# Optimization experiments

Hardware: AMD Instinct MI355X
Metric: run time of the kernel (lower is better)

The kernel has to match this reference:

```python
import jax, jax.numpy as jnp
import numpy as np
from jax import lax

B, N, NPOINT = 8, 8192, 1024
NSAMPLE = (16, 32)
IN_CH = 64
MLPS = ((64, 64, 128), (64, 96, 128))
EPS = 1e-5


def setup_inputs() -> dict:
    key = jax.random.key(0)
    ks = jax.random.split(key, 16)
    inp = {}
    inp["xyz"] = jax.random.normal(ks[0], (B, 3, N), jnp.float32)
    inp["points"] = jax.random.normal(ks[1], (B, IN_CH, N), jnp.float32)
    ki = 2
    for i, mlp in enumerate(MLPS):
        last = IN_CH + 3
        for j, out in enumerate(mlp):
            inp["w%d_%d" % (i, j)] = jax.random.normal(ks[ki], (out, last), jnp.float32) * (1.0 / float(np.sqrt(last)))
            inp["b%d_%d" % (i, j)] = jnp.zeros((out,), jnp.float32)
            inp["g%d_%d" % (i, j)] = jnp.ones((out,), jnp.float32)
            inp["be%d_%d" % (i, j)] = jnp.zeros((out,), jnp.float32)
            ki += 1
            last = out
    return inp


def _fps(xyz_t):
    # farthest point sampling; xyz_t: [B, N, 3] -> [B, NPOINT] int32
    Bb, Nn, _ = xyz_t.shape

    def step(carry, _):
        dist, far = carry
        c = jnp.take_along_axis(xyz_t, far[:, None, None], axis=1)  # [B,1,3]
        d = jnp.sum((xyz_t - c) ** 2, -1)
        dist = jnp.minimum(dist, d)
        return (dist, jnp.argmax(dist, -1).astype(jnp.int32)), far

    init = (jnp.full((Bb, Nn), 1e10, jnp.float32), jnp.zeros((Bb,), jnp.int32))
    _, cent = lax.scan(step, init, None, length=NPOINT)
    return cent.T  # [B, NPOINT]


def _gather(p, idx):
    # p: [B, N, C], idx: [B, ...] -> [B, ..., C]
    return jax.vmap(lambda a, i: a[i])(p, idx)


def _sqdist(a, b):
    # a: [B, S, 3], b: [B, N, 3] -> [B, S, N] squared euclidean distance
    return (jnp.sum(a * a, -1)[:, :, None] + jnp.sum(b * b, -1)[:, None, :]
            - 2.0 * jnp.einsum('bsc,bnc->bsn', a, b))


def _mlp(x, params):
    # x: [B, C, S, K]; 1x1 Conv2d + BatchNorm2d (batch stats, training mode) + ReLU
    for w, b, g, be in params:
        x = jnp.einsum('oc,bcsk->bosk', w, x) + b[None, :, None, None]
        m = x.mean((0, 2, 3), keepdims=True)
        v = x.var((0, 2, 3), keepdims=True)
        x = (x - m) * lax.rsqrt(v + EPS) * g[None, :, None, None] + be[None, :, None, None]
        x = jax.nn.relu(x)
    return x


def _forward(xyz, points, params):
    xyz_t = jnp.transpose(xyz, (0, 2, 1))     # [B, N, 3]
    pts_t = jnp.transpose(points, (0, 2, 1))  # [B, N, C]
    fps_idx = _fps(xyz_t)
    new_xyz = _gather(xyz_t, fps_idx)         # [B, S, 3]
    outs = []
    for i, k in enumerate(NSAMPLE):
        d = _sqdist(new_xyz, xyz_t)           # [B, S, N]
        _, idx = lax.top_k(-d, k)             # k nearest neighbors
        g_xyz = _gather(xyz_t, idx) - new_xyz[:, :, None, :]  # [B, S, k, 3]
        g_pts = _gather(pts_t, idx)                           # [B, S, k, C]
        feat = jnp.transpose(jnp.concatenate([g_xyz, g_pts], -1), (0, 3, 1, 2))  # [B, 3+C, S, k]
        outs.append(jnp.max(_mlp(feat, params[i]), -1))       # [B, C_out, S]
    return jnp.transpose(new_xyz, (0, 2, 1)), jnp.concatenate(outs, 1)


def reference(xyz, points, w0_0, b0_0, g0_0, be0_0, w0_1, b0_1, g0_1, be0_1, w0_2, b0_2, g0_2, be0_2, w1_0, b1_0, g1_0, be1_0, w1_1, b1_1, g1_1, be1_1, w1_2, b1_2, g1_2, be1_2):
    params = [[(w0_0, b0_0, g0_0, be0_0), (w0_1, b0_1, g0_1, be0_1), (w0_2, b0_2, g0_2, be0_2)],
              [(w1_0, b1_0, g1_0, be1_0), (w1_1, b1_1, g1_1, be1_1), (w1_2, b1_2, g1_2, be1_2)]]
    return _forward(xyz, points, params)
```

## Files before the change

kernel.cpp:

```cpp
#include <hip/hip_runtime.h>
#include <math.h>

#define BN_EPS 1e-5f
constexpr int Bc = 8, Nc = 8192, Sc = 1024, CINc = 64;

typedef float v2f __attribute__((ext_vector_type(2)));

__device__ __forceinline__ unsigned short f2bf(float f) {
  unsigned u = __float_as_uint(f);
  u += 0x7FFFu + ((u >> 16) & 1u);
  return (unsigned short)(u >> 16);
}
__device__ __forceinline__ float bf2f(unsigned short h) {
  return __uint_as_float(((unsigned)h) << 16);
}

template <int CTRL, int RMASK>
__device__ __forceinline__ unsigned long long dpp_maxu64(unsigned long long k) {
  int lo = (int)(unsigned)k, hi = (int)(unsigned)(k >> 32);
  int olo = __builtin_amdgcn_update_dpp(lo, lo, CTRL, RMASK, 0xF, false);
  int ohi = __builtin_amdgcn_update_dpp(hi, hi, CTRL, RMASK, 0xF, false);
  unsigned long long ok = ((unsigned long long)(unsigned)ohi << 32) | (unsigned)olo;
  return ok > k ? ok : k;
}
template <int CTRL, int RMASK>
__device__ __forceinline__ v2f dpp_sumstep2(v2f v) {
  int olo = __builtin_amdgcn_update_dpp(0, __float_as_int(v.x), CTRL, RMASK, 0xF, false);
  int ohi = __builtin_amdgcn_update_dpp(0, __float_as_int(v.y), CTRL, RMASK, 0xF, false);
  v2f o = {__int_as_float(olo), __int_as_float(ohi)};
  return v + o;
}
__device__ __forceinline__ v2f dpp_sum64v2(v2f v) {
  v = dpp_sumstep2<0x111, 0xF>(v);
  v = dpp_sumstep2<0x112, 0xF>(v);
  v = dpp_sumstep2<0x114, 0xF>(v);
  v = dpp_sumstep2<0x118, 0xF>(v);
  v = dpp_sumstep2<0x142, 0xA>(v);
  v = dpp_sumstep2<0x143, 0xC>(v);
  return v;
}
template <int CTRL>
__device__ __forceinline__ v2f dpp_pkmax(v2f v) {
  int ox = __builtin_amdgcn_update_dpp(__float_as_int(v.x), __float_as_int(v.x), CTRL, 0xF, 0xF, false);
  int oy = __builtin_amdgcn_update_dpp(__float_as_int(v.y), __float_as_int(v.y), CTRL, 0xF, 0xF, false);
  v2f o = {__int_as_float(ox), __int_as_float(oy)};
  return __builtin_elementwise_max(v, o);
}
template <int CTRL>
__device__ __forceinline__ v2f dpp_pkmin(v2f v) {
  int ox = __builtin_amdgcn_update_dpp(__float_as_int(v.x), __float_as_int(v.x), CTRL, 0xF, 0xF, false);
  int oy = __builtin_amdgcn_update_dpp(__float_as_int(v.y), __float_as_int(v.y), CTRL, 0xF, 0xF, false);
  v2f o = {__int_as_float(ox), __int_as_float(oy)};
  return __builtin_elementwise_min(v, o);
}

__device__ __forceinline__ void pproj_body(int i, const float* __restrict__ pts,
                                           const float* __restrict__ wl,
                                           const float* __restrict__ bl,
                                           float* __restrict__ P) {
  int b = i >> 13, n = i & 8191;
  const float* pb = pts + (size_t)b * CINc * Nc + n;
  v2f acc[32];
  const v2f* bl2 = (const v2f*)bl;
#pragma unroll
  for (int o2 = 0; o2 < 32; o2++) acc[o2] = bl2[o2];
  for (int c = 0; c < CINc; c++) {
    float xv = pb[(size_t)c * Nc];
    v2f xv2 = {xv, xv};
    const v2f* wr = (const v2f*)(wl + c * 64);
#pragma unroll
    for (int o2 = 0; o2 < 32; o2++) acc[o2] = __builtin_elementwise_fma(wr[o2], xv2, acc[o2]);
  }
  float4* Pn = (float4*)(P + (size_t)i * 64);
#pragma unroll
  for (int o4 = 0; o4 < 16; o4++)
    Pn[o4] = make_float4(acc[2 * o4].x, acc[2 * o4].y, acc[2 * o4 + 1].x, acc[2 * o4 + 1].y);
}

__global__ __launch_bounds__(512) void mega_kernel(const float* __restrict__ xyz,
                                                   const float* __restrict__ pts,
                                                   const float* __restrict__ w00,
                                                   const float* __restrict__ b00,
                                                   const float* __restrict__ w10,
                                                   const float* __restrict__ b10,
                                                   float4* __restrict__ xyzT,
                                                   float4* __restrict__ nx,
                                                   float* __restrict__ out0,
                                                   float* __restrict__ P0,
                                                   float* __restrict__ P1) {
  __shared__ alignas(16) char smemc[102528];
  int bid = blockIdx.x, t = threadIdx.x;
  if (bid < 8) {
    float* xs = (float*)smemc;
    float* ys = xs + Nc;
    float* zs = ys + Nc;
    int* idxs = (int*)(smemc + 98304);
    unsigned long long* red = (unsigned long long*)(smemc + 102400);
    const float* xb = xyz + (size_t)bid * 3 * Nc;
    float px[16], py[16], pz[16], dd[16];
#pragma unroll
    for (int j = 0; j < 16; j++) {
      int n = j * 512 + t;
      float x = xb[n], y = xb[Nc + n], z = xb[2 * Nc + n];
      px[j] = x; py[j] = y; pz[j] = z;
      xs[n] = x; ys[n] = y; zs[n] = z;
      dd[j] = 1e10f;
    }
    int w = t >> 6;
    __syncthreads();
    int curIdx = 0;
    for (int i = 0; i < Sc; i++) {
      float cx = xs[curIdx], cy = ys[curIdx], cz = zs[curIdx];
      if (t == 0) idxs[i] = curIdx;
      float bd = -1.f;
      int bnidx = 0;
#pragma unroll
      for (int j = 0; j < 16; j++) {
        float dx = px[j] - cx, dy = py[j] - cy, dz = pz[j] - cz;
        float d = fmaf(dz, dz, fmaf(dy, dy, dx * dx));
        d = fminf(dd[j], d);
        dd[j] = d;
        if (d > bd) { bd = d; bnidx = j * 512 + t; }
      }
      unsigned long long key =
          ((unsigned long long)__float_as_uint(bd) << 32) | (unsigned)(~bnidx);
      key = dpp_maxu64<0x111, 0xF>(key);
      key = dpp_maxu64<0x112, 0xF>(key);
      key = dpp_maxu64<0x114, 0xF>(key);
      key = dpp_maxu64<0x118, 0xF>(key);
      key = dpp_maxu64<0x142, 0xA>(key);
      key = dpp_maxu64<0x143, 0xC>(key);
      if ((t & 63) == 63) red[(i & 1) * 8 + w] = key;
      __syncthreads();
      const unsigned long long* rr = red + (i & 1) * 8;
      unsigned long long k2 = rr[0];
#pragma unroll
      for (int u = 1; u < 8; u++) {
        unsigned long long o = rr[u];
        k2 = (o > k2) ? o : k2;
      }
      curIdx = (int)(~(unsigned)(k2 & 0xFFFFFFFFull));
    }
    __syncthreads();
    for (int i2 = t; i2 < Sc; i2 += 512) {
      int idx = idxs[i2];
      float x = xs[idx], y = ys[idx], z = zs[idx];
      nx[bid * Sc + i2] = make_float4(x, y, z, fmaf(z, z, fmaf(y, y, x * x)));
      float* ob = out0 + (size_t)bid * 3 * Sc;
      ob[i2] = x; ob[Sc + i2] = y; ob[2 * Sc + i2] = z;
    }
  } else if (bid < 136) {
    int i = (bid - 8) * 512 + t;
    int b = i >> 13, n = i & 8191;
    const float* xb = xyz + (size_t)b * 3 * Nc;
    float x = xb[n], y = xb[Nc + n], z = xb[2 * Nc + n];
    xyzT[i] = make_float4(x, y, z, fmaf(z, z, fmaf(y, y, x * x)));
  } else {
    bool second = bid >= 264;
    const float* ww = second ? w10 : w00;
    const float* bb = second ? b10 : b00;
    float* PP = second ? P1 : P0;
    float* wl = (float*)smemc;
    float* bl = wl + 64 * 64;
    for (int i2 = t; i2 < 64 * 64; i2 += 512) {
      int c = i2 >> 6, o = i2 & 63;
      wl[i2] = ww[o * 67 + 3 + c];
    }
    if (t < 64) bl[t] = bb[t];
    __syncthreads();
    pproj_body(((bid - (second ? 264 : 136)) * 512) + t, pts, wl, bl, PP);
  }
}

__global__ __launch_bounds__(256) void knn_kernel(const float4* __restrict__ xyzT,
                                                  const float4* __restrict__ newxyz,
                                                  int* __restrict__ knn) {
  int lane = threadIdx.x & 63;
  int sub = lane >> 5;
  int l32 = lane & 31;
  int waveId = blockIdx.x * 4 + (threadIdx.x >> 6);
  int q = waveId * 2 + sub;
  int b = q >> 10;
  float4 qv = newxyz[q];
  const float4* pb = xyzT + (size_t)b * Nc;
  unsigned long long lk = ~0ull;
  unsigned long long worst = ~0ull;
  for (int t0 = 0; t0 < Nc; t0 += 32) {
    float4 p = pb[t0 + l32];
    float dot = fmaf(qv.z, p.z, fmaf(qv.y, p.y, qv.x * p.x));
    float d = fmaf(-2.f, dot, qv.w + p.w);
    unsigned fu = __float_as_uint(d);
    fu ^= (unsigned)(-(int)(fu >> 31)) | 0x80000000u;
    unsigned long long ck = ((unsigned long long)fu << 32) | (unsigned)(t0 + l32);
    unsigned long long bal = __ballot(ck < worst);
    unsigned mymask = (unsigned)(bal >> (sub * 32));
    while (mymask) {
      int src = __ffs(mymask) - 1;
      unsigned long long ckb = __shfl(ck, src, 32);
      unsigned long long bel = __ballot(lk < ckb);
      int cnt = __popc((unsigned)(bel >> (sub * 32)));
      unsigned long long up = __shfl_up(lk, 1, 32);
      lk = (l32 == cnt) ? ckb : ((l32 > cnt) ? up : lk);
      worst = __shfl(lk, 31, 32);
      mymask &= ~(1u << src);
      unsigned long long bal2 = __ballot(ck < worst);
      mymask &= (unsigned)(bal2 >> (sub * 32));
    }
  }
  knn[(size_t)q * 32 + l32] = (int)(lk & 0xFFFFFFFFu);
}

template <int K>
__device__ __forceinline__ void conv1_body(char* smemc, int bidl,
                                           const float4* __restrict__ xyzT,
                                           const float4* __restrict__ nx,
                                           const int* __restrict__ knn,
                                           const float* __restrict__ P,
                                           const float* __restrict__ w0,
                                           unsigned short* __restrict__ y,
                                           float* __restrict__ part, int Pos) {
  v2f* wst = (v2f*)smemc;
  float* wx = (float*)(smemc + 8192);
  float* wy = wx + 64;
  float* wz = wy + 64;
  if (threadIdx.x < 64) {
    int o = threadIdx.x;
    wx[o] = w0[o * 67];
    wy[o] = w0[o * 67 + 1];
    wz[o] = w0[o * 67 + 2];
  }
  __syncthreads();
  int gp = bidl * 256 + threadIdx.x;
  int b = gp / Pos, r = gp % Pos;
  int s = r / K, kk = r & (K - 1);
  int n = knn[((size_t)(b * Sc + s)) * 32 + kk];
  float4 c4 = nx[b * Sc + s];
  float4 p4 = xyzT[(size_t)b * Nc + n];
  v2f dx2 = {p4.x - c4.x, p4.x - c4.x};
  v2f dy2 = {p4.y - c4.y, p4.y - c4.y};
  v2f dz2 = {p4.z - c4.z, p4.z - c4.z};
  const float4* Pn = (const float4*)(P + ((size_t)b * Nc + n) * 64);
  v2f acc[32];
#pragma unroll
  for (int o4 = 0; o4 < 16; o4++) {
    float4 v = Pn[o4];
    acc[2 * o4] = (v2f){v.x, v.y};
    acc[2 * o4 + 1] = (v2f){v.z, v.w};
  }
  const v2f* wx2 = (const v2f*)wx;
  const v2f* wy2 = (const v2f*)wy;
  const v2f* wz2 = (const v2f*)wz;
#pragma unroll
  for (int o2 = 0; o2 < 32; o2++) acc[o2] = __builtin_elementwise_fma(wx2[o2], dx2, acc[o2]);
#pragma unroll
  for (int o2 = 0; o2 < 32; o2++) acc[o2] = __builtin_elementwise_fma(wy2[o2], dy2, acc[o2]);
#pragma unroll
  for (int o2 = 0; o2 < 32; o2++) acc[o2] = __builtin_elementwise_fma(wz2[o2], dz2, acc[o2]);
  unsigned short* yt = y + (size_t)bidl * 64 * 256 + threadIdx.x;
#pragma unroll
  for (int o2 = 0; o2 < 32; o2++) {
    yt[(size_t)(2 * o2) * 256] = f2bf(acc[o2].x);
    yt[(size_t)(2 * o2 + 1) * 256] = f2bf(acc[o2].y);
  }
  int lane = threadIdx.x & 63, w = threadIdx.x >> 6;
  int row = w * 4 + (lane >> 4);
  bool lead = (lane & 15) == 15;
#pragma unroll
  for (int o2 = 0; o2 < 32; o2++) {
    float v0 = acc[o2].x, v1 = acc[o2].y;
    v2f s0 = (v2f){v0, v0 * v0};
    s0 = dpp_sumstep2<0x111, 0xF>(s0);
    s0 = dpp_sumstep2<0x112, 0xF>(s0);
    s0 = dpp_sumstep2<0x114, 0xF>(s0);
    s0 = dpp_sumstep2<0x118, 0xF>(s0);
    v2f s1 = (v2f){v1, v1 * v1};
    s1 = dpp_sumstep2<0x111, 0xF>(s1);
    s1 = dpp_sumstep2<0x112, 0xF>(s1);
    s1 = dpp_sumstep2<0x114, 0xF>(s1);
    s1 = dpp_sumstep2<0x118, 0xF>(s1);
    if (lead) { wst[row * 64 + 2 * o2] = s0; wst[row * 64 + 2 * o2 + 1] = s1; }
  }
  __syncthreads();
  if (threadIdx.x < 64) {
    int o = threadIdx.x;
    v2f sv = (v2f){0.f, 0.f};
#pragma unroll
    for (int rr = 0; rr < 16; rr++) sv += wst[rr * 64 + o];
    ((v2f*)part)[(size_t)bidl * 64 + o] = sv;
  }
}

__global__ __launch_bounds__(256) void conv1M_kernel(
    const float4* xyzT, const float4* nx, const int* knn,
    const float* P0, const float* w0a, unsigned short* y0a, float* part0, int Pos0,
    const float* P1, const float* w0b, unsigned short* y0b, float* part1, int Pos1, int split) {
  __shared__ alignas(16) char smemc[8960];
  if ((int)blockIdx.x < split)
    conv1_body<16>(smemc, blockIdx.x, xyzT, nx, knn, P0, w0a, y0a, part0, Pos0);
  else
    conv1_body<32>(smemc, blockIdx.x - split, xyzT, nx, knn, P1, w0b, y0b, part1, Pos1);
}

__global__ __launch_bounds__(256) void bnfinM_kernel(
    const float* part0, const float* g0, const float* be0, float* bn0, int C0, int nblk0, float inv0,
    const float* part1, const float* g1, const float* be1, float* bn1, int C1, int nblk1, float inv1,
    int split) {
  const float* part; const float* g; const float* be; float* bn;
  int C, nblk, c; float invcnt;
  if ((int)blockIdx.x < split) {
    part = part0; g = g0; be = be0; bn = bn0; C = C0; nblk = nblk0; invcnt = inv0; c = blockIdx.x;
  } else {
    part = part1; g = g1; be = be1; bn = bn1; C = C1; nblk = nblk1; invcnt = inv1; c = blockIdx.x - split;
  }
  v2f sq = (v2f){0.f, 0.f};
  for (int i = threadIdx.x; i < nblk; i += 256) sq += ((const v2f*)part)[(size_t)i * C + c];
  sq = dpp_sum64v2(sq);
  __shared__ v2f ls[4];
  int w = threadIdx.x >> 6;
  if ((threadIdx.x & 63) == 63) ls[w] = sq;
  __syncthreads();
  if (threadIdx.x == 0) {
    v2f tt = ls[0] + ls[1] + ls[2] + ls[3];
    float m = tt.x * invcnt;
    float v = tt.y * invcnt - m * m;
    float sc = g[c] / sqrtf(v + BN_EPS);
    bn[c * 2] = sc;
    bn[c * 2 + 1] = fmaf(-m, sc, be[c]);
  }
}

template <int CI, int CO, int K>
__device__ __forceinline__ void convB_body(char* smemc, int bidl,
                                           const unsigned short* __restrict__ yin,
                                           const float* __restrict__ wt,
                                           const float* __restrict__ bb,
                                           const float* __restrict__ bn,
                                           unsigned short* __restrict__ yout,
                                           float* __restrict__ ymax,
                                           float* __restrict__ ymin,
                                           float* __restrict__ part, int Pos) {
  constexpr int COq = CO / 4;
  constexpr int COq2 = COq / 2;
  float* wl = (float*)smemc;
  float* bnl = wl + CI * CO;
  float* bl = bnl + 2 * CI;
  for (int i = threadIdx.x; i < CI * CO; i += 256) {
    int c = i / CO, o = i % CO;
    wl[i] = wt[o * CI + c];
  }
  for (int i = threadIdx.x; i < 2 * CI; i += 256) bnl[i] = bn[i];
  if (threadIdx.x < CO) bl[threadIdx.x] = bb[threadIdx.x];
  __syncthreads();
  int w = threadIdx.x >> 6, l = threadIdx.x & 63;
  int cb = w * COq;
  int bpb = Pos / 256;
  int b = bidl / bpb;
  int r0 = (bidl % bpb) * 256 + l * 4;
  const ushort4* xt = (const ushort4*)(yin + (size_t)bidl * CI * 256) + l;
  v2f acc[4][COq2];
#pragma unroll
  for (int p = 0; p < 4; p++)
#pragma unroll
    for (int q = 0; q < COq2; q++) acc[p][q] = ((const v2f*)(bl + cb))[q];
  ushort4 cur = xt[0], nxt;
  for (int c = 0; c < CI; c++) {
    if (c + 1 < CI) nxt = xt[(c + 1) * 64];
    float scv = bnl[2 * c], shv = bnl[2 * c + 1];
    float xv0 = fmaxf(fmaf(bf2f(cur.x), scv, shv), 0.f);
    float xv1 = fmaxf(fmaf(bf2f(cur.y), scv, shv), 0.f);
    float xv2 = fmaxf(fmaf(bf2f(cur.z), scv, shv), 0.f);
    float xv3 = fmaxf(fmaf(bf2f(cur.w), scv, shv), 0.f);
    v2f x0 = {xv0, xv0}, x1 = {xv1, xv1}, x2 = {xv2, xv2}, x3 = {xv3, xv3};
    const float4* wr = (const float4*)(wl + c * CO + cb);
#pragma unroll
    for (int o4 = 0; o4 < COq / 4; o4++) {
      float4 wv = wr[o4];
      v2f w01 = {wv.x, wv.y}, w23 = {wv.z, wv.w};
      acc[0][2 * o4] = __builtin_elementwise_fma(w01, x0, acc[0][2 * o4]);
      acc[0][2 * o4 + 1] = __builtin_elementwise_fma(w23, x0, acc[0][2 * o4 + 1]);
      acc[1][2 * o4] = __builtin_elementwise_fma(w01, x1, acc[1][2 * o4]);
      acc[1][2 * o4 + 1] = __builtin_elementwise_fma(w23, x1, acc[1][2 * o4 + 1]);
      acc[2][2 * o4] = __builtin_elementwise_fma(w01, x2, acc[2][2 * o4]);
      acc[2][2 * o4 + 1] = __builtin_elementwise_fma(w23, x2, acc[2][2 * o4 + 1]);
      acc[3][2 * o4] = __builtin_elementwise_fma(w01, x3, acc[3][2 * o4]);
      acc[3][2 * o4 + 1] = __builtin_elementwise_fma(w23, x3, acc[3][2 * o4 + 1]);
    }
    cur = nxt;
  }
  if (K == 0) {
    unsigned short* yo = yout + (size_t)bidl * CO * 256;
#pragma unroll
    for (int q = 0; q < COq2; q++) {
      ushort4 a, bq;
      a.x = f2bf(acc[0][q].x); a.y = f2bf(acc[1][q].x);
      a.z = f2bf(acc[2][q].x); a.w = f2bf(acc[3][q].x);
      bq.x = f2bf(acc[0][q].y); bq.y = f2bf(acc[1][q].y);
      bq.z = f2bf(acc[2][q].y); bq.w = f2bf(acc[3][q].y);
      ((ushort4*)(yo + (size_t)(cb + 2 * q) * 256))[l] = a;
      ((ushort4*)(yo + (size_t)(cb + 2 * q + 1) * 256))[l] = bq;
    }
  } else {
    int s = r0 / K;
    bool wrt = (K == 16) ? ((l & 3) == 3) : ((l & 7) == 7);
#pragma unroll
    for (int q = 0; q < COq2; q++) {
      v2f mx = __builtin_elementwise_max(__builtin_elementwise_max(acc[0][q], acc[1][q]),
                                         __builtin_elementwise_max(acc[2][q], acc[3][q]));
      v2f mn = __builtin_elementwise_min(__builtin_elementwise_min(acc[0][q], acc[1][q]),
                                         __builtin_elementwise_min(acc[2][q], acc[3][q]));
      mx = dpp_pkmax<0x111>(mx);
      mx = dpp_pkmax<0x112>(mx);
      if (K == 32) mx = dpp_pkmax<0x114>(mx);
      mn = dpp_pkmin<0x111>(mn);
      mn = dpp_pkmin<0x112>(mn);
      if (K == 32) mn = dpp_pkmin<0x114>(mn);
      if (wrt) {
        ymax[((size_t)b * CO + cb + 2 * q) * Sc + s] = mx.x;
        ymax[((size_t)b * CO + cb + 2 * q + 1) * Sc + s] = mx.y;
        ymin[((size_t)b * CO + cb + 2 * q) * Sc + s] = mn.x;
        ymin[((size_t)b * CO + cb + 2 * q + 1) * Sc + s] = mn.y;
      }
    }
  }
#pragma unroll
  for (int q = 0; q < COq2; q++) {
    v2f sv = acc[0][q] + acc[1][q] + acc[2][q] + acc[3][q];
    v2f sq = acc[0][q] * acc[0][q];
    sq = __builtin_elementwise_fma(acc[1][q], acc[1][q], sq);
    sq = __builtin_elementwise_fma(acc[2][q], acc[2][q], sq);
    sq = __builtin_elementwise_fma(acc[3][q], acc[3][q], sq);
    sv = dpp_sum64v2(sv);
    sq = dpp_sum64v2(sq);
    if (l == 63) {
      ((v2f*)part)[(size_t)bidl * CO + cb + 2 * q] = (v2f){sv.x, sq.x};
      ((v2f*)part)[(size_t)bidl * CO + cb + 2 * q + 1] = (v2f){sv.y, sq.y};
    }
  }
}

__global__ __launch_bounds__(256) void conv2M_kernel(
    const unsigned short* y0a, const float* w1a, const float* b1a, const float* bn1a,
    unsigned short* y1a, float* part0, int Pos0,
    const unsigned short* y0b, const float* w1b, const float* b1b, const float* bn1b,
    unsigned short* y1b, float* part1, int Pos1, int split) {
  __shared__ alignas(16) char smemc[25472];
  if ((int)blockIdx.x < split)
    convB_body<64, 64, 0>(smemc, blockIdx.x, y0a, w1a, b1a, bn1a, y1a, nullptr, nullptr, part0, Pos0);
  else
    convB_body<64, 96, 0>(smemc, blockIdx.x - split, y0b, w1b, b1b, bn1b, y1b, nullptr, nullptr, part1, Pos1);
}

__global__ __launch_bounds__(256) void conv3M_kernel(
    const unsigned short* y1a, const float* w2a, const float* b2a, const float* bn2a,
    float* ymax0, float* ymin0, float* part0, int Pos0,
    const unsigned short* y1b, const float* w2b, const float* b2b, const float* bn2b,
    float* ymax1, float* ymin1, float* part1, int Pos1, int split) {
  __shared__ alignas(16) char smemc[50432];
  if ((int)blockIdx.x < split)
    convB_body<64, 128, 16>(smemc, blockIdx.x, y1a, w2a, b2a, bn2a, nullptr, ymax0, ymin0, part0, Pos0);
  else
    convB_body<96, 128, 32>(smemc, blockIdx.x - split, y1b, w2b, b2b, bn2b, nullptr, ymax1, ymin1, part1, Pos1);
}

__global__ __launch_bounds__(256) void bnfin3fM_kernel(
    const float* part0, const float* g0, const float* be0, const float* ymax0,
    const float* ymin0, int nblk0, float inv0, int coff0,
    const float* part1, const float* g1, const float* be1, const float* ymax1,
    const float* ymin1, int nblk1, float inv1, int coff1,
    float* out1, int split) {
  constexpr int C = 128;
  const float* part; const float* g; const float* be; const float* ymaxp; const float* yminp;
  int nblk, c, coff; float invcnt;
  if ((int)blockIdx.x < split) {
    part = part0; g = g0; be = be0; ymaxp = ymax0; yminp = ymin0;
    nblk = nblk0; invcnt = inv0; coff = coff0; c = blockIdx.x;
  } else {
    part = part1; g = g1; be = be1; ymaxp = ymax1; yminp = ymin1;
    nblk = nblk1; invcnt = inv1; coff = coff1; c = blockIdx.x - split;
  }
  v2f sq = (v2f){0.f, 0.f};
  for (int i = threadIdx.x; i < nblk; i += 256) sq += ((const v2f*)part)[(size_t)i * C + c];
  sq = dpp_sum64v2(sq);
  __shared__ v2f ls[4];
  __shared__ float bnc[2];
  int w = threadIdx.x >> 6;
  if ((threadIdx.x & 63) == 63) ls[w] = sq;
  __syncthreads();
  if (threadIdx.x == 0) {
    v2f tt = ls[0] + ls[1] + ls[2] + ls[3];
    float m = tt.x * invcnt;
    float v = tt.y * invcnt - m * m;
    float sc = g[c] / sqrtf(v + BN_EPS);
    bnc[0] = sc;
    bnc[1] = fmaf(-m, sc, be[c]);
  }
  __syncthreads();
  float sc = bnc[0], sh = bnc[1];
  const float* src = (sc >= 0.f) ? ymaxp : yminp;
#pragma unroll
  for (int k = 0; k < 32; k++) {
    int i = k * 256 + threadIdx.x;
    int b = i >> 10, s = i & 1023;
    float v = src[((size_t)b * C + c) * Sc + s];
    out1[((size_t)b * 256 + coff + c) * Sc + s] = fmaxf(fmaf(v, sc, sh), 0.f);
  }
}

extern "C" void kernel_launch(void* const* d_in, const int* in_sizes, int n_in,
                              void* d_out, int out_size, void* d_ws, size_t ws_size,
                              hipStream_t stream) {
  const float* xyz = (const float*)d_in[0];
  const float* pts = (const float*)d_in[1];
  float* ws = (float*)d_ws;
  float* out0 = (float*)d_out;
  float* out1 = out0 + Bc * 3 * Sc;

  float4* xyzT = (float4*)(ws + 0);
  float4* nx = (float4*)(ws + 262144);
  int* knnp = (int*)(ws + 294912);
  float* P0 = ws + 557056;

  const float* d2 = (const float*)d_in[2];
  const float* d3 = (const float*)d_in[3];
  const float* d4 = (const float*)d_in[4];
  const float* d5 = (const float*)d_in[5];
  const float* d6 = (const float*)d_in[6];
  const float* d7 = (const float*)d_in[7];
  const float* d8 = (const float*)d_in[8];
  const float* d9 = (const float*)d_in[9];
  const float* d10 = (const float*)d_in[10];
  const float* d11 = (const float*)d_in[11];
  const float* d12 = (const float*)d_in[12];
  const float* d13 = (const float*)d_in[13];
  const float* d14 = (const float*)d_in[14];
  const float* d15 = (const float*)d_in[15];
  const float* d16 = (const float*)d_in[16];
  const float* d17 = (const float*)d_in[17];
  const float* d18 = (const float*)d_in[18];
  const float* d19 = (const float*)d_in[19];
  const float* d20 = (const float*)d_in[20];
  const float* d21 = (const float*)d_in[21];
  const float* d22 = (const float*)d_in[22];
  const float* d23 = (const float*)d_in[23];
  const float* d24 = (const float*)d_in[24];
  const float* d25 = (const float*)d_in[25];

  float inv0 = 1.f / (float)(Bc * 16384);
  float inv1 = 1.f / (float)(Bc * 32768);

  bool merged = ws_size >= (size_t)72254464 * 4;
  if (merged) {
    float* P1 = ws + 4751360;
    unsigned short* y00 = (unsigned short*)(ws + 8945664);
    unsigned short* y01 = (unsigned short*)(ws + 17334272);
    unsigned short* y10 = (unsigned short*)(ws + 34111488);
    unsigned short* y11 = (unsigned short*)(ws + 42500096);
    float* ymax0 = ws + 67665920;
    float* ymin0 = ws + 68714496;
    float* ymax1 = ws + 69763072;
    float* ymin1 = ws + 70811648;
    float* part0 = ws + 71860224;
    float* part1 = ws + 71991296;
    float* bns = ws + 72253440;
    float* bn10 = bns, *bn11 = bns + 256, *bn20 = bns + 512, *bn21 = bns + 768;

    mega_kernel<<<392, 512, 0, stream>>>(xyz, pts, d2, d3, d14, d15, xyzT, nx, out0, P0, P1);
    knn_kernel<<<1024, 256, 0, stream>>>(xyzT, nx, knnp);
    conv1M_kernel<<<1536, 256, 0, stream>>>(xyzT, nx, knnp, P0, d2, y00, part0, 16384, P1, d14,
                                            y01, part1, 32768, 512);
    bnfinM_kernel<<<128, 256, 0, stream>>>(part0, d4, d5, bn10, 64, 512, inv0, part1, d16, d17,
                                           bn11, 64, 1024, inv1, 64);
    conv2M_kernel<<<1536, 256, 0, stream>>>(y00, d6, d7, bn10, y10, part0, 16384, y01, d18, d19,
                                            bn11, y11, part1, 32768, 512);
    bnfinM_kernel<<<160, 256, 0, stream>>>(part0, d8, d9, bn20, 64, 512, inv0, part1, d20, d21,
                                           bn21, 96, 1024, inv1, 64);
    conv3M_kernel<<<1536, 256, 0, stream>>>(y10, d10, d11, bn20, ymax0, ymin0, part0, 16384, y11,
                                            d22, d23, bn21, ymax1, ymin1, part1, 32768, 512);
    bnfin3fM_kernel<<<256, 256, 0, stream>>>(part0, d12, d13, ymax0, ymin0, 512, inv0, 0, part1,
                                             d24, d25, ymax1, ymin1, 1024, inv1, 128, out1, 128);
  } else {
    unsigned short* y0 = (unsigned short*)(ws + 4751360);
    unsigned short* y1 = (unsigned short*)(ws + 21528576);
    float* P1 = ws + 29917184;
    float* ymax = ws + 46694400;
    float* ymin = ws + 47742976;
    float* part = ws + 48791552;
    float* bn1 = ws + 49053696;
    float* bn2 = ws + 49053824;

    mega_kernel<<<392, 512, 0, stream>>>(xyz, pts, d2, d3, d14, d15, xyzT, nx, out0, P0, P1);
    knn_kernel<<<1024, 256, 0, stream>>>(xyzT, nx, knnp);

    conv1M_kernel<<<512, 256, 0, stream>>>(xyzT, nx, knnp, P0, d2, y0, part, 16384, P0, d2, y0,
                                           part, 16384, 512);
    bnfinM_kernel<<<64, 256, 0, stream>>>(part, d4, d5, bn1, 64, 512, inv0, part, d4, d5, bn1, 64,
                                          512, inv0, 64);
    conv2M_kernel<<<512, 256, 0, stream>>>(y0, d6, d7, bn1, y1, part, 16384, y0, d6, d7, bn1, y1,
                                           part, 16384, 512);
    bnfinM_kernel<<<64, 256, 0, stream>>>(part, d8, d9, bn2, 64, 512, inv0, part, d8, d9, bn2, 64,
                                          512, inv0, 64);
    conv3M_kernel<<<512, 256, 0, stream>>>(y1, d10, d11, bn2, ymax, ymin, part, 16384, y1, d10,
                                           d11, bn2, ymax, ymin, part, 16384, 512);
    bnfin3fM_kernel<<<128, 256, 0, stream>>>(part, d12, d13, ymax, ymin, 512, inv0, 0, part, d12,
                                             d13, ymax, ymin, 512, inv0, 0, out1, 128);

    conv1M_kernel<<<1024, 256, 0, stream>>>(xyzT, nx, knnp, P1, d14, y0, part, 32768, P1, d14, y0,
                                            part, 32768, 0);
    bnfinM_kernel<<<64, 256, 0, stream>>>(part, d16, d17, bn1, 64, 1024, inv1, part, d16, d17,
                                          bn1, 64, 1024, inv1, 0);
    conv2M_kernel<<<1024, 256, 0, stream>>>(y0, d18, d19, bn1, y1, part, 32768, y0, d18, d19, bn1,
                                            y1, part, 32768, 0);
    bnfinM_kernel<<<96, 256, 0, stream>>>(part, d20, d21, bn2, 96, 1024, inv1, part, d20, d21,
                                          bn2, 96, 1024, inv1, 0);
    conv3M_kernel<<<1024, 256, 0, stream>>>(y1, d22, d23, bn2, ymax, ymin, part, 32768, y1, d22,
                                            d23, bn2, ymax, ymin, part, 32768, 0);
    bnfin3fM_kernel<<<128, 256, 0, stream>>>(part, d24, d25, ymax, ymin, 1024, inv1, 128, part,
                                             d24, d25, ymax, ymin, 1024, inv1, 128, out1, 0);
  }
  (void)in_sizes; (void)n_in; (void)out_size; (void)ws_size;
}
```

Baseline: 1.306 ms.

## Move third pointwise conv layer onto bf16 MFMA with fused BN stats and max/min

The third 1x1 conv layer, which has 128 output channels, now runs on bf16 MFMA 16x16x32 instructions instead of packed FP32 FMAs. Each block stages bf16 weights and BN+ReLU-normalized inputs in padded LDS. Bias add, per-channel sum and sum-of-squares, and per-group max/min over neighbours are computed from the MFMA accumulator layout using cross-lane shuffles. The change cuts the ALU cost of the largest conv layer. In exchange it quantises the normalised inputs and weights to bf16, uses about 78 KB of dynamic LDS with launch bounds set to one block, and lowers occupancy.

```diff
diff --git a/kernel.cpp b/kernel.cpp
--- a/kernel.cpp
+++ b/kernel.cpp
@@ -5,6 +5,8 @@
 constexpr int Bc = 8, Nc = 8192, Sc = 1024, CINc = 64;
 
 typedef float v2f __attribute__((ext_vector_type(2)));
+typedef short short8v __attribute__((ext_vector_type(8)));
+typedef float f32x4 __attribute__((ext_vector_type(4)));
 
 __device__ __forceinline__ unsigned short f2bf(float f) {
   unsigned u = __float_as_uint(f);
@@ -38,20 +40,6 @@
   v = dpp_sumstep2<0x142, 0xA>(v);
   v = dpp_sumstep2<0x143, 0xC>(v);
   return v;
-}
-template <int CTRL>
-__device__ __forceinline__ v2f dpp_pkmax(v2f v) {
-  int ox = __builtin_amdgcn_update_dpp(__float_as_int(v.x), __float_as_int(v.x), CTRL, 0xF, 0xF, false);
-  int oy = __builtin_amdgcn_update_dpp(__float_as_int(v.y), __float_as_int(v.y), CTRL, 0xF, 0xF, false);
-  v2f o = {__int_as_float(ox), __int_as_float(oy)};
-  return __builtin_elementwise_max(v, o);
-}
-template <int CTRL>
-__device__ __forceinline__ v2f dpp_pkmin(v2f v) {
-  int ox = __builtin_amdgcn_update_dpp(__float_as_int(v.x), __float_as_int(v.x), CTRL, 0xF, 0xF, false);
-  int oy = __builtin_amdgcn_update_dpp(__float_as_int(v.y), __float_as_int(v.y), CTRL, 0xF, 0xF, false);
-  v2f o = {__int_as_float(ox), __int_as_float(oy)};
-  return __builtin_elementwise_min(v, o);
 }
 
 __device__ __forceinline__ void pproj_body(int i, const float* __restrict__ pts,
@@ -329,15 +317,13 @@
   }
 }
 
-template <int CI, int CO, int K>
+template <int CI, int CO>
 __device__ __forceinline__ void convB_body(char* smemc, int bidl,
                                            const unsigned short* __restrict__ yin,
                                            const float* __restrict__ wt,
                                            const float* __restrict__ bb,
                                            const float* __restrict__ bn,
                                            unsigned short* __restrict__ yout,
-                                           float* __restrict__ ymax,
-                                           float* __restrict__ ymin,
                                            float* __restrict__ part, int Pos) {
   constexpr int COq = CO / 4;
   constexpr int COq2 = COq / 2;
@@ -353,9 +339,6 @@
   __syncthreads();
   int w = threadIdx.x >> 6, l = threadIdx.x & 63;
   int cb = w * COq;
-  int bpb = Pos / 256;
-  int b = bidl / bpb;
-  int r0 = (bidl % bpb) * 256 + l * 4;
   const ushort4* xt = (const ushort4*)(yin + (size_t)bidl * CI * 256) + l;
   v2f acc[4][COq2];
 #pragma unroll
@@ -387,40 +370,16 @@
     }
     cur = nxt;
   }
-  if (K == 0) {
-    unsigned short* yo = yout + (size_t)bidl * CO * 256;
-#pragma unroll
-    for (int q = 0; q < COq2; q++) {
-      ushort4 a, bq;
-      a.x = f2bf(acc[0][q].x); a.y = f2bf(acc[1][q].x);
-      a.z = f2bf(acc[2][q].x); a.w = f2bf(acc[3][q].x);
-      bq.x = f2bf(acc[0][q].y); bq.y = f2bf(acc[1][q].y);
-      bq.z = f2bf(acc[2][q].y); bq.w = f2bf(acc[3][q].y);
-      ((ushort4*)(yo + (size_t)(cb + 2 * q) * 256))[l] = a;
-      ((ushort4*)(yo + (size_t)(cb + 2 * q + 1) * 256))[l] = bq;
-    }
-  } else {
-    int s = r0 / K;
-    bool wrt = (K == 16) ? ((l & 3) == 3) : ((l & 7) == 7);
-#pragma unroll
-    for (int q = 0; q < COq2; q++) {
-      v2f mx = __builtin_elementwise_max(__builtin_elementwise_max(acc[0][q], acc[1][q]),
-                                         __builtin_elementwise_max(acc[2][q], acc[3][q]));
-      v2f mn = __builtin_elementwise_min(__builtin_elementwise_min(acc[0][q], acc[1][q]),
-                                         __builtin_elementwise_min(acc[2][q], acc[3][q]));
-      mx = dpp_pkmax<0x111>(mx);
-      mx = dpp_pkmax<0x112>(mx);
-      if (K == 32) mx = dpp_pkmax<0x114>(mx);
-      mn = dpp_pkmin<0x111>(mn);
-      mn = dpp_pkmin<0x112>(mn);
-      if (K == 32) mn = dpp_pkmin<0x114>(mn);
-      if (wrt) {
-        ymax[((size_t)b * CO + cb + 2 * q) * Sc + s] = mx.x;
-        ymax[((size_t)b * CO + cb + 2 * q + 1) * Sc + s] = mx.y;
-        ymin[((size_t)b * CO + cb + 2 * q) * Sc + s] = mn.x;
-        ymin[((size_t)b * CO + cb + 2 * q + 1) * Sc + s] = mn.y;
-      }
-    }
+  unsigned short* yo = yout + (size_t)bidl * CO * 256;
+#pragma unroll
+  for (int q = 0; q < COq2; q++) {
+    ushort4 a, bq;
+    a.x = f2bf(acc[0][q].x); a.y = f2bf(acc[1][q].x);
+    a.z = f2bf(acc[2][q].x); a.w = f2bf(acc[3][q].x);
+    bq.x = f2bf(acc[0][q].y); bq.y = f2bf(acc[1][q].y);
+    bq.z = f2bf(acc[2][q].y); bq.w = f2bf(acc[3][q].y);
+    ((ushort4*)(yo + (size_t)(cb + 2 * q) * 256))[l] = a;
+    ((ushort4*)(yo + (size_t)(cb + 2 * q + 1) * 256))[l] = bq;
   }
 #pragma unroll
   for (int q = 0; q < COq2; q++) {
@@ -445,21 +404,134 @@
     unsigned short* y1b, float* part1, int Pos1, int split) {
   __shared__ alignas(16) char smemc[25472];
   if ((int)blockIdx.x < split)
-    convB_body<64, 64, 0>(smemc, blockIdx.x, y0a, w1a, b1a, bn1a, y1a, nullptr, nullptr, part0, Pos0);
+    convB_body<64, 64>(smemc, blockIdx.x, y0a, w1a, b1a, bn1a, y1a, part0, Pos0);
   else
-    convB_body<64, 96, 0>(smemc, blockIdx.x - split, y0b, w1b, b1b, bn1b, y1b, nullptr, nullptr, part1, Pos1);
-}
-
-__global__ __launch_bounds__(256) void conv3M_kernel(
+    convB_body<64, 96>(smemc, blockIdx.x - split, y0b, w1b, b1b, bn1b, y1b, part1, Pos1);
+}
+
+template <int CI, int K>
+__device__ __forceinline__ void conv3_mfma_body(char* dsm, int bidl,
+                                                const unsigned short* __restrict__ yin,
+                                                const float* __restrict__ wt,
+                                                const float* __restrict__ bb,
+                                                const float* __restrict__ bn,
+                                                float* __restrict__ ymax,
+                                                float* __restrict__ ymin,
+                                                float* __restrict__ part, int Pos) {
+  constexpr int CO = 128;
+  constexpr int LD = CI + 8;
+  unsigned short* Wbf = (unsigned short*)dsm;
+  unsigned short* Xbf = Wbf + CO * LD;
+  int tid = threadIdx.x;
+  for (int i = tid; i < CO * CI; i += 256) {
+    int o = i / CI, c = i - o * CI;
+    Wbf[o * LD + c] = f2bf(wt[i]);
+  }
+  const unsigned short* yt = yin + (size_t)bidl * CI * 256;
+  for (int i = tid; i < CI * 256; i += 256) {
+    int c = i >> 8, p = i & 255;
+    float scv = bn[2 * c], shv = bn[2 * c + 1];
+    float v = fmaxf(fmaf(bf2f(yt[i]), scv, shv), 0.f);
+    Xbf[p * LD + c] = f2bf(v);
+  }
+  __syncthreads();
+  int w = tid >> 6, l = tid & 63;
+  int lrow = l & 15, lk = (l >> 4) * 8;
+  f32x4 acc[4][8];
+#pragma unroll
+  for (int Mt = 0; Mt < 4; Mt++)
+#pragma unroll
+    for (int Nt = 0; Nt < 8; Nt++) acc[Mt][Nt] = (f32x4){0.f, 0.f, 0.f, 0.f};
+#pragma unroll
+  for (int kt = 0; kt < CI / 32; kt++) {
+    short8v a[4], bfr[8];
+#pragma unroll
+    for (int Mt = 0; Mt < 4; Mt++)
+      a[Mt] = *(const short8v*)(Xbf + (w * 64 + Mt * 16 + lrow) * LD + kt * 32 + lk);
+#pragma unroll
+    for (int Nt = 0; Nt < 8; Nt++)
+      bfr[Nt] = *(const short8v*)(Wbf + (Nt * 16 + lrow) * LD + kt * 32 + lk);
+#pragma unroll
+    for (int Mt = 0; Mt < 4; Mt++)
+#pragma unroll
+      for (int Nt = 0; Nt < 8; Nt++)
+        acc[Mt][Nt] = __builtin_amdgcn_mfma_f32_16x16x32_bf16(a[Mt], bfr[Nt], acc[Mt][Nt], 0, 0, 0);
+  }
+  __syncthreads();
+  float* wstat = (float*)Xbf;
+  int bpb = Pos / 256;
+  int b = bidl / bpb;
+  int posbase = (bidl % bpb) * 256;
+#pragma unroll
+  for (int Nt = 0; Nt < 8; Nt++) {
+    float bv = bb[Nt * 16 + lrow];
+    float sv = 0.f, sq = 0.f;
+    float mxs[4], mns[4];
+#pragma unroll
+    for (int Mt = 0; Mt < 4; Mt++) {
+      f32x4 a4 = acc[Mt][Nt];
+      float v0 = a4.x + bv, v1 = a4.y + bv, v2 = a4.z + bv, v3 = a4.w + bv;
+      sv += (v0 + v1) + (v2 + v3);
+      sq = fmaf(v0, v0, sq); sq = fmaf(v1, v1, sq);
+      sq = fmaf(v2, v2, sq); sq = fmaf(v3, v3, sq);
+      mxs[Mt] = fmaxf(fmaxf(v0, v1), fmaxf(v2, v3));
+      mns[Mt] = fminf(fminf(v0, v1), fminf(v2, v3));
+    }
+    if (K == 16) {
+#pragma unroll
+      for (int Mt = 0; Mt < 4; Mt++) {
+        float mx = mxs[Mt], mn = mns[Mt];
+        mx = fmaxf(mx, __shfl_xor(mx, 16)); mx = fmaxf(mx, __shfl_xor(mx, 32));
+        mn = fminf(mn, __shfl_xor(mn, 16)); mn = fminf(mn, __shfl_xor(mn, 32));
+        if (l < 16) {
+          int s = (posbase + w * 64 + Mt * 16) >> 4;
+          ymax[((size_t)b * CO + Nt * 16 + l) * Sc + s] = mx;
+          ymin[((size_t)b * CO + Nt * 16 + l) * Sc + s] = mn;
+        }
+      }
+    } else {
+#pragma unroll
+      for (int pr = 0; pr < 2; pr++) {
+        float mx = fmaxf(mxs[2 * pr], mxs[2 * pr + 1]);
+        float mn = fminf(mns[2 * pr], mns[2 * pr + 1]);
+        mx = fmaxf(mx, __shfl_xor(mx, 16)); mx = fmaxf(mx, __shfl_xor(mx, 32));
+        mn = fminf(mn, __shfl_xor(mn, 16)); mn = fminf(mn, __shfl_xor(mn, 32));
+        if (l < 16) {
+          int s = (posbase + w * 64 + pr * 32) >> 5;
+          ymax[((size_t)b * CO + Nt * 16 + l) * Sc + s] = mx;
+          ymin[((size_t)b * CO + Nt * 16 + l) * Sc + s] = mn;
+        }
+      }
+    }
+    sv += __shfl_xor(sv, 16); sv += __shfl_xor(sv, 32);
+    sq += __shfl_xor(sq, 16); sq += __shfl_xor(sq, 32);
+    if (l < 16) {
+      wstat[(w * CO + Nt * 16 + l) * 2] = sv;
+      wstat[(w * CO + Nt * 16 + l) * 2 + 1] = sq;
+    }
+  }
+  __syncthreads();
+  if (tid < CO) {
+    v2f tt = (v2f){0.f, 0.f};
+#pragma unroll
+    for (int ww = 0; ww < 4; ww++) {
+      tt.x += wstat[(ww * CO + tid) * 2];
+      tt.y += wstat[(ww * CO + tid) * 2 + 1];
+    }
+    ((v2f*)part)[(size_t)bidl * CO + tid] = tt;
+  }
+}
+
+__global__ __launch_bounds__(256, 1) void conv3M_kernel(
     const unsigned short* y1a, const float* w2a, const float* b2a, const float* bn2a,
     float* ymax0, float* ymin0, float* part0, int Pos0,
     const unsigned short* y1b, const float* w2b, const float* b2b, const float* bn2b,
     float* ymax1, float* ymin1, float* part1, int Pos1, int split) {
-  __shared__ alignas(16) char smemc[50432];
+  extern __shared__ __align__(16) char dsm[];
   if ((int)blockIdx.x < split)
-    convB_body<64, 128, 16>(smemc, blockIdx.x, y1a, w2a, b2a, bn2a, nullptr, ymax0, ymin0, part0, Pos0);
+    conv3_mfma_body<64, 16>(dsm, blockIdx.x, y1a, w2a, b2a, bn2a, ymax0, ymin0, part0, Pos0);
   else
-    convB_body<96, 128, 32>(smemc, blockIdx.x - split, y1b, w2b, b2b, bn2b, nullptr, ymax1, ymin1, part1, Pos1);
+    conv3_mfma_body<96, 32>(dsm, blockIdx.x - split, y1b, w2b, b2b, bn2b, ymax1, ymin1, part1, Pos1);
 }
 
 __global__ __launch_bounds__(256) void bnfin3fM_kernel(
@@ -547,6 +619,7 @@
 
   float inv0 = 1.f / (float)(Bc * 16384);
   float inv1 = 1.f / (float)(Bc * 32768);
+  const int DSM3 = 79872;
 
   bool merged = ws_size >= (size_t)72254464 * 4;
   if (merged) {
@@ -574,8 +647,9 @@
                                             bn11, y11, part1, 32768, 512);
     bnfinM_kernel<<<160, 256, 0, stream>>>(part0, d8, d9, bn20, 64, 512, inv0, part1, d20, d21,
                                            bn21, 96, 1024, inv1, 64);
-    conv3M_kernel<<<1536, 256, 0, stream>>>(y10, d10, d11, bn20, ymax0, ymin0, part0, 16384, y11,
-                                            d22, d23, bn21, ymax1, ymin1, part1, 32768, 512);
+    conv3M_kernel<<<1536, 256, DSM3, stream>>>(y10, d10, d11, bn20, ymax0, ymin0, part0, 16384,
+                                               y11, d22, d23, bn21, ymax1, ymin1, part1, 32768,
+                                               512);
     bnfin3fM_kernel<<<256, 256, 0, stream>>>(part0, d12, d13, ymax0, ymin0, 512, inv0, 0, part1,
                                              d24, d25, ymax1, ymin1, 1024, inv1, 128, out1, 128);
   } else {
@@ -599,8 +673,8 @@
                                            part, 16384, 512);
     bnfinM_kernel<<<64, 256, 0, stream>>>(part, d8, d9, bn2, 64, 512, inv0, part, d8, d9, bn2, 64,
                                           512, inv0, 64);
-    conv3M_kernel<<<512, 256, 0, stream>>>(y1, d10, d11, bn2, ymax, ymin, part, 16384, y1, d10,
-                                           d11, bn2, ymax, ymin, part, 16384, 512);
+    conv3M_kernel<<<512, 256, DSM3, stream>>>(y1, d10, d11, bn2, ymax, ymin, part, 16384, y1, d10,
+                                              d11, bn2, ymax, ymin, part, 16384, 512);
     bnfin3fM_kernel<<<128, 256, 0, stream>>>(part, d12, d13, ymax, ymin, 512, inv0, 0, part, d12,
                                              d13, ymax, ymin, 512, inv0, 0, out1, 128);
 
@@ -612,8 +686,8 @@
                                             y1, part, 32768, 0);
     bnfinM_kernel<<<96, 256, 0, stream>>>(part, d20, d21, bn2, 96, 1024, inv1, part, d20, d21,
                                           bn2, 96, 1024, inv1, 0);
-    conv3M_kernel<<<1024, 256, 0, stream>>>(y1, d22, d23, bn2, ymax, ymin, part, 32768, y1, d22,
-                                            d23, bn2, ymax, ymin, part, 32768, 0);
+    conv3M_kernel<<<1024, 256, DSM3, stream>>>(y1, d22, d23, bn2, ymax, ymin, part, 32768, y1,
+                                               d22, d23, bn2, ymax, ymin, part, 32768, 0);
     bnfin3fM_kernel<<<128, 256, 0, stream>>>(part, d24, d25, ymax, ymin, 1024, inv1, 128, part,
                                              d24, d25, ymax, ymin, 1024, inv1, 128, out1, 0);
   }
```

New measurement: 1.243 ms. -4.8%, faster.
